# Performance work log

Measured on AMD Instinct MI355X. Metric: run time of the kernel, lower is better.

The kernel has to match this reference:

```python
import jax, jax.numpy as jnp
import numpy as np

DIM = 256
QK_DIM = 256
SCALE = QK_DIM ** (-0.5)


def depthwise_conv3x3(x_img, w, b):
    # x_img: [B, C, H, W], w: [C, 1, 3, 3] (OIHW, groups=C), b: [C]
    out = jax.lax.conv_general_dilated(
        x_img, w, window_strides=(1, 1), padding='SAME',
        feature_group_count=x_img.shape[1],
        dimension_numbers=('NCHW', 'OIHW', 'NCHW'))
    return out + b[None, :, None, None]


def setup_inputs() -> dict:
    key = jax.random.key(0)
    ks = jax.random.split(key, 7)
    B, N, C = 4, 4096, DIM
    s = 0.02
    return {
        'x': jax.random.normal(ks[0], (B, N, C), jnp.float32),
        'W_qkv': jax.random.normal(ks[1], (C, 3 * C), jnp.float32) * s,
        'W_gate': jax.random.normal(ks[2], (C, C), jnp.float32) * s,
        'b_gate': jax.random.normal(ks[3], (C,), jnp.float32) * s,
        'W_proj': jax.random.normal(ks[4], (C, C), jnp.float32) * s,
        'pe_w': jax.random.normal(ks[5], (C, 1, 3, 3), jnp.float32) * s,
        'pe_b': jax.random.normal(ks[6], (C,), jnp.float32) * s,
    }


def reference(x, W_qkv, W_gate, b_gate, W_proj, pe_w, pe_b):
    B, N, C = x.shape
    ws = int(N ** 0.5)
    qkv = x @ W_qkv                               # [B, N, 3C]
    q, k, v = jnp.split(qkv, [QK_DIM, 2 * QK_DIM], axis=-1)
    z = jax.nn.gelu(x @ W_gate + b_gate, approximate=False)  # [B, N, C]
    # depthwise-conv positional encoding on q viewed as an image
    q_img = jnp.transpose(q, (0, 2, 1)).reshape(B, C, ws, ws)
    pe = depthwise_conv3x3(q_img, pe_w, pe_b).reshape(B, C, N)
    pe = jnp.transpose(pe, (0, 2, 1))             # [B, N, C]
    # single-head attention (heads arg unused in the original forward)
    attn = jax.nn.softmax(jnp.einsum('bnc,bmc->bnm', q, k) * SCALE, axis=-1)
    out = jnp.einsum('bnm,bmc->bnc', attn, v) + pe
    out = out * z
    return out @ W_proj
```

## Files before the change

### kernel.cpp

```cpp
#include <hip/hip_runtime.h>
#include <hip/hip_bf16.h>
#include <math.h>
#include <stdint.h>

typedef unsigned short u16;
typedef __attribute__((ext_vector_type(8))) short bf8;
typedef __attribute__((ext_vector_type(4))) float f4;

#define SC_LOG2E 0.09016844f

__device__ __forceinline__ float b2f(u16 u) {
    union { uint32_t i; float f; } v; v.i = ((uint32_t)u) << 16; return v.f;
}
__device__ __forceinline__ u16 f2b(float f) {
    union { float f; uint32_t i; } v; v.f = f;
    uint32_t r = (v.i + 0x7FFFu + ((v.i >> 16) & 1u)) >> 16;
    return (u16)r;
}
__device__ __forceinline__ uint32_t pk_bf16(float lo, float hi) {
    uint32_t r;
    asm("v_cvt_pk_bf16_f32 %0, %1, %2" : "=v"(r) : "v"(lo), "v"(hi));
    return r;
}

__global__ __launch_bounds__(256) void prep_all(
        const float* __restrict__ Wqkv, const float* __restrict__ Wgate,
        const float* __restrict__ Wproj, const float* __restrict__ x,
        u16* __restrict__ WT_all, u16* __restrict__ WTp,
        u16* __restrict__ xb) {
    int bid = blockIdx.x;
    if (bid < 80) {
        __shared__ float tile[64][65];
        int t = threadIdx.x;
        int lid = (bid < 64) ? bid : (bid - 64);
        int n0 = (lid >> 2) * 64, k0 = (lid & 3) * 64;
        const float* src; int stride, ncol; u16* dst;
        if (bid < 64) {
            if (n0 < 768) { src = Wqkv; stride = 768; ncol = n0; }
            else          { src = Wgate; stride = 256; ncol = n0 - 768; }
            dst = WT_all;
        } else { src = Wproj; stride = 256; ncol = n0; dst = WTp; }
        int cr = t & 63, rr = t >> 6;
#pragma unroll
        for (int i = 0; i < 16; i++) {
            int r = rr * 16 + i;
            tile[r][cr] = src[(size_t)(k0 + r) * stride + ncol + cr];
        }
        __syncthreads();
#pragma unroll
        for (int i = 0; i < 16; i++) {
            int rw = rr * 16 + i;
            dst[(size_t)(n0 + rw) * 256 + k0 + cr] = f2b(tile[cr][rw]);
        }
    } else {
        int i = ((bid - 80) * 256 + threadIdx.x) * 4;
        float4 f = *(const float4*)&x[i];
        uint2 o;
        o.x = pk_bf16(f.x, f.y);
        o.y = pk_bf16(f.z, f.w);
        *(uint2*)&xb[i] = o;
    }
}

__global__ __launch_bounds__(512) void gemm_qkvz(
        const u16* __restrict__ xb, const u16* __restrict__ WT,
        const float* __restrict__ b_gate,
        u16* __restrict__ qo, u16* __restrict__ ko,
        u16* __restrict__ vT, u16* __restrict__ zo) {
    __shared__ u16 As[64 * 520];
    __shared__ u16 Bp[2][32 * 520];
    const int t = threadIdx.x;
    const int w = t >> 6, lane = t & 63, l15 = lane & 15, q4 = lane >> 4;
    const int m0 = blockIdx.x * 128;
    const int nb = blockIdx.y * 512;

    const int lo = lane >> 5;
    const int lcn = ((lane & 31) - 4 * lo) & 31;

    auto stageA = [&]() {
#pragma unroll
        for (int rr = 0; rr < 8; rr++) {
            int pp = rr * 8 + w;
            const u16* g = &xb[(size_t)(m0 + pp * 2 + lo) * 256 + lcn * 8];
            __builtin_amdgcn_global_load_lds(
                (const __attribute__((address_space(1))) unsigned int*)g,
                (__attribute__((address_space(3))) unsigned int*)&As[pp * 520],
                16, 0, 0);
        }
    };
    auto stageB = [&](int p, u16* dst) {
#pragma unroll
        for (int rr = 0; rr < 4; rr++) {
            int pp = rr * 8 + w;
            const u16* g = &WT[(size_t)(nb + p * 64 + pp * 2 + lo) * 256 + lcn * 8];
            __builtin_amdgcn_global_load_lds(
                (const __attribute__((address_space(1))) unsigned int*)g,
                (__attribute__((address_space(3))) unsigned int*)&dst[pp * 520],
                16, 0, 0);
        }
    };
    auto kaddr = [&](const u16* base, int row, int cn) -> const u16* {
        int o = row & 1;
        return base + (row >> 1) * 520 + o * 256 + (((cn + 4 * o) & 31) << 3);
    };

    stageA();
    stageB(0, Bp[0]);

    const int mtb = (w & 3) * 32;
    const int ntb = (w >> 2) * 32;

    for (int p = 0; p < 8; ++p) {
        __syncthreads();
        if (p < 7) stageB(p + 1, Bp[(p + 1) & 1]);
        const u16* Bs = Bp[p & 1];
        const int n0g = nb + p * 64;
        const int kind = n0g >> 8;
        const int pcol = n0g & 255;

        f4 acc[2][2];
#pragma unroll
        for (int i = 0; i < 2; i++)
#pragma unroll
            for (int j = 0; j < 2; j++) acc[i][j] = (f4){0.f, 0.f, 0.f, 0.f};

        __builtin_amdgcn_s_setprio(1);
#pragma unroll
        for (int c = 0; c < 8; c++) {
            bf8 af0 = *(const bf8*)kaddr(As, mtb + l15, c * 4 + q4);
            bf8 af1 = *(const bf8*)kaddr(As, mtb + 16 + l15, c * 4 + q4);
            bf8 bf0 = *(const bf8*)kaddr(Bs, ntb + l15, c * 4 + q4);
            bf8 bf1 = *(const bf8*)kaddr(Bs, ntb + 16 + l15, c * 4 + q4);
            if (kind == 2) {
                acc[0][0] = __builtin_amdgcn_mfma_f32_16x16x32_bf16(af0, bf0, acc[0][0], 0, 0, 0);
                acc[0][1] = __builtin_amdgcn_mfma_f32_16x16x32_bf16(af0, bf1, acc[0][1], 0, 0, 0);
                acc[1][0] = __builtin_amdgcn_mfma_f32_16x16x32_bf16(af1, bf0, acc[1][0], 0, 0, 0);
                acc[1][1] = __builtin_amdgcn_mfma_f32_16x16x32_bf16(af1, bf1, acc[1][1], 0, 0, 0);
            } else {
                acc[0][0] = __builtin_amdgcn_mfma_f32_16x16x32_bf16(bf0, af0, acc[0][0], 0, 0, 0);
                acc[0][1] = __builtin_amdgcn_mfma_f32_16x16x32_bf16(bf1, af0, acc[0][1], 0, 0, 0);
                acc[1][0] = __builtin_amdgcn_mfma_f32_16x16x32_bf16(bf0, af1, acc[1][0], 0, 0, 0);
                acc[1][1] = __builtin_amdgcn_mfma_f32_16x16x32_bf16(bf1, af1, acc[1][1], 0, 0, 0);
            }
        }
        __builtin_amdgcn_s_setprio(0);

        if (kind == 2) {
            int bb = m0 >> 12;
            int nnb = (m0 & 4095) + mtb + q4 * 4;
#pragma unroll
            for (int i = 0; i < 2; i++) {
                int nn = nnb + i * 16;
#pragma unroll
                for (int j = 0; j < 2; j++) {
                    int vc = pcol + ntb + j * 16 + l15;
                    uint2 pk;
                    pk.x = pk_bf16(acc[i][j][0], acc[i][j][1]);
                    pk.y = pk_bf16(acc[i][j][2], acc[i][j][3]);
                    *(uint2*)&vT[(size_t)(bb * 256 + vc) * 4096 + nn] = pk;
                }
            }
        } else if (kind == 3) {
#pragma unroll
            for (int i = 0; i < 2; i++) {
                size_t mrow = (size_t)(m0 + mtb + i * 16 + l15) * 256 + pcol;
#pragma unroll
                for (int j = 0; j < 2; j++) {
                    int col = ntb + j * 16 + q4 * 4;
                    float4 bg4 = *(const float4*)&b_gate[pcol + col];
                    float v0 = acc[i][j][0] + bg4.x;
                    float v1 = acc[i][j][1] + bg4.y;
                    float v2 = acc[i][j][2] + bg4.z;
                    float v3 = acc[i][j][3] + bg4.w;
                    v0 = 0.5f * v0 * (1.0f + erff(v0 * 0.70710678118654752f));
                    v1 = 0.5f * v1 * (1.0f + erff(v1 * 0.70710678118654752f));
                    v2 = 0.5f * v2 * (1.0f + erff(v2 * 0.70710678118654752f));
                    v3 = 0.5f * v3 * (1.0f + erff(v3 * 0.70710678118654752f));
                    uint2 o;
                    o.x = pk_bf16(v0, v1);
                    o.y = pk_bf16(v2, v3);
                    *(uint2*)&zo[mrow + col] = o;
                }
            }
        } else {
            u16* dst = (kind == 0) ? qo : ko;
#pragma unroll
            for (int i = 0; i < 2; i++) {
                size_t mrow = (size_t)(m0 + mtb + i * 16 + l15) * 256 + pcol;
#pragma unroll
                for (int j = 0; j < 2; j++) {
                    int col = ntb + j * 16 + q4 * 4;
                    uint2 o;
                    o.x = pk_bf16(acc[i][j][0], acc[i][j][1]);
                    o.y = pk_bf16(acc[i][j][2], acc[i][j][3]);
                    *(uint2*)&dst[mrow + col] = o;
                }
            }
        }
    }
}

__global__ __launch_bounds__(256) void conv_pe(
        const u16* __restrict__ q, const float* __restrict__ pw,
        const float* __restrict__ pb, u16* __restrict__ pe) {
    const int bid = blockIdx.x;
    const int b = bid >> 8, h = (bid >> 2) & 63, wsg = bid & 3;
    const int t = threadIdx.x;
    const int c4 = (t & 63) * 4;
    const int ws4 = t >> 6;
    const int w0 = wsg * 16 + ws4 * 4;

    float wf[36];
#pragma unroll
    for (int j = 0; j < 9; j++) {
        float4 v = *(const float4*)&pw[c4 * 9 + j * 4];
        wf[j * 4 + 0] = v.x; wf[j * 4 + 1] = v.y;
        wf[j * 4 + 2] = v.z; wf[j * 4 + 3] = v.w;
    }
    float4 bias4 = *(const float4*)&pb[c4];
    float bias[4] = {bias4.x, bias4.y, bias4.z, bias4.w};

    const u16* qb = q + b * (4096 * 256);
    u16* peb = pe + b * (4096 * 256);
    const bool vTop = h > 0, vBot = h < 63;

    float v[3][6][4];
#pragma unroll
    for (int j = 0; j < 6; j++) {
        int pos = w0 - 1 + j;
        bool inw = (pos >= 0) && (pos < 64);
#pragma unroll
        for (int r = 0; r < 3; r++) {
            bool ok = inw && ((r == 0) ? vTop : (r == 2) ? vBot : true);
            ushort4 u4 = {0, 0, 0, 0};
            if (ok) u4 = *(const ushort4*)&qb[((h - 1 + r) * 64 + pos) * 256 + c4];
            v[r][j][0] = b2f(u4.x); v[r][j][1] = b2f(u4.y);
            v[r][j][2] = b2f(u4.z); v[r][j][3] = b2f(u4.w);
        }
    }
#pragma unroll
    for (int w2 = 0; w2 < 4; w2++) {
        float o[4];
#pragma unroll
        for (int ch = 0; ch < 4; ch++) {
            float acc = bias[ch];
#pragma unroll
            for (int r = 0; r < 3; r++)
#pragma unroll
                for (int j = 0; j < 3; j++)
                    acc += wf[ch * 9 + r * 3 + j] * v[r][w2 + j][ch];
            o[ch] = acc;
        }
        uint2 st;
        st.x = pk_bf16(o[0], o[1]);
        st.y = pk_bf16(o[2], o[3]);
        *(uint2*)&peb[(h * 64 + w0 + w2) * 256 + c4] = st;
    }
}

__global__ __launch_bounds__(512) void attn(
        const u16* __restrict__ q, const u16* __restrict__ k,
        const u16* __restrict__ vT, const u16* __restrict__ pe,
        const u16* __restrict__ z, const u16* __restrict__ WTp,
        float* __restrict__ out) {
    __shared__ u16 Kst[32 * 520];
    __shared__ u16 Vs2[2][256 * 64];
    __shared__ u16 Ps[64 * 72];
    __shared__ float l_part[8][64];

    const int t = threadIdx.x;
    const int w = t >> 6, lane = t & 63, l15 = lane & 15, q4 = lane >> 4;
    const int kg = w >> 1, qh = w & 1;
    const int xcd = blockIdx.x & 7;
    const int b = xcd >> 1;
    const int qt = (blockIdx.x >> 3) * 2 + (xcd & 1);
    const int m0 = b * 4096 + qt * 64;

    const u16* kb = k + (size_t)b * 4096 * 256;
    const u16* vbase = vT + (size_t)b * 256 * 4096;

    const int lo = lane >> 5;
    const int lcn = ((lane & 31) - 4 * lo) & 31;

    auto stage64 = [&](const u16* src) {
#pragma unroll
        for (int rr = 0; rr < 4; rr++) {
            int pp = rr * 8 + w;
            const u16* g = src + (size_t)(pp * 2 + lo) * 256 + lcn * 8;
            u16* l = &Kst[pp * 520];
            __builtin_amdgcn_global_load_lds(
                (const __attribute__((address_space(1))) unsigned int*)g,
                (__attribute__((address_space(3))) unsigned int*)l, 16, 0, 0);
        }
    };
    const int vrl = lane >> 3, vsl = lane & 7;
    auto stageV = [&](const u16* src, u16* dst) {
#pragma unroll
        for (int j = 0; j < 4; j++) {
            int op = j * 8 + w;
            int r = op * 8 + vrl;
            int cn = (vsl - r) & 7;
            const u16* g = src + (size_t)r * 4096 + cn * 8;
            u16* l = dst + op * 512;
            __builtin_amdgcn_global_load_lds(
                (const __attribute__((address_space(1))) unsigned int*)g,
                (__attribute__((address_space(3))) unsigned int*)l, 16, 0, 0);
        }
    };
    auto kaddr = [&](int row, int cn) -> const u16* {
        int o = row & 1;
        return &Kst[(row >> 1) * 520 + o * 256 + (((cn + 4 * o) & 31) << 3)];
    };

    stage64(q + (size_t)m0 * 256);
    __syncthreads();
    bf8 qf[2][8];
#pragma unroll
    for (int qtt = 0; qtt < 2; qtt++)
#pragma unroll
        for (int c = 0; c < 8; c++)
            qf[qtt][c] = *(const bf8*)kaddr(qh * 32 + qtt * 16 + l15, c * 4 + q4);
    __syncthreads();

    stage64(kb);
    stageV(vbase, Vs2[0]);

    f4 O[2][4];
#pragma unroll
    for (int vg = 0; vg < 2; vg++)
#pragma unroll
        for (int qg = 0; qg < 4; qg++) O[vg][qg] = (f4){0.f, 0.f, 0.f, 0.f};
    float lrow[2] = {0.f, 0.f};

    auto body = [&](int kt, const u16* Vcur, u16* Vnxt) {
        __syncthreads();

        f4 St[2];
        St[0] = (f4){0.f, 0.f, 0.f, 0.f};
        St[1] = (f4){0.f, 0.f, 0.f, 0.f};
        __builtin_amdgcn_s_setprio(1);
#pragma unroll
        for (int c = 0; c < 8; c++) {
            bf8 kf = *(const bf8*)kaddr(kg * 16 + l15, c * 4 + q4);
            St[0] = __builtin_amdgcn_mfma_f32_16x16x32_bf16(kf, qf[0][c], St[0], 0, 0, 0);
            St[1] = __builtin_amdgcn_mfma_f32_16x16x32_bf16(kf, qf[1][c], St[1], 0, 0, 0);
        }
        __builtin_amdgcn_s_setprio(0);

#pragma unroll
        for (int qtt = 0; qtt < 2; qtt++) {
            float e0 = exp2f(fminf(fmaxf(St[qtt][0] * SC_LOG2E, -30.f), 30.f));
            float e1 = exp2f(fminf(fmaxf(St[qtt][1] * SC_LOG2E, -30.f), 30.f));
            float e2 = exp2f(fminf(fmaxf(St[qtt][2] * SC_LOG2E, -30.f), 30.f));
            float e3 = exp2f(fminf(fmaxf(St[qtt][3] * SC_LOG2E, -30.f), 30.f));
            uint2 pk;
            pk.x = pk_bf16(e0, e1);
            pk.y = pk_bf16(e2, e3);
            int qrow = qh * 32 + qtt * 16 + l15;
            *(uint2*)&Ps[qrow * 72 + kg * 16 + q4 * 4] = pk;
            float s = (e0 + e1) + (e2 + e3);
            s += __shfl_xor(s, 16);
            s += __shfl_xor(s, 32);
            lrow[qtt] += s;
        }
        __syncthreads();

        if (kt < 63) {
            stage64(kb + (size_t)(kt + 1) * 16384);
            stageV(vbase + (size_t)(kt + 1) * 64, Vnxt);
        }

        bf8 pf[4][2], vfr[2][2];
#pragma unroll
        for (int qg = 0; qg < 4; qg++)
#pragma unroll
            for (int kh = 0; kh < 2; kh++)
                pf[qg][kh] = *(bf8*)&Ps[(qg * 16 + l15) * 72 + kh * 32 + q4 * 8];
#pragma unroll
        for (int vg = 0; vg < 2; vg++)
#pragma unroll
            for (int kh = 0; kh < 2; kh++) {
                int R = w * 32 + vg * 16 + l15;
                int slot = ((kh * 4 + q4) + R) & 7;
                vfr[vg][kh] = *(const bf8*)&Vcur[R * 64 + slot * 8];
            }
        __builtin_amdgcn_s_setprio(1);
#pragma unroll
        for (int vg = 0; vg < 2; vg++)
#pragma unroll
            for (int qg = 0; qg < 4; qg++) {
                O[vg][qg] = __builtin_amdgcn_mfma_f32_16x16x32_bf16(
                    vfr[vg][0], pf[qg][0], O[vg][qg], 0, 0, 0);
                O[vg][qg] = __builtin_amdgcn_mfma_f32_16x16x32_bf16(
                    vfr[vg][1], pf[qg][1], O[vg][qg], 0, 0, 0);
            }
        __builtin_amdgcn_s_setprio(0);
    };

    for (int kt2 = 0; kt2 < 64; kt2 += 2) {
        body(kt2,     Vs2[0], Vs2[1]);
        body(kt2 + 1, Vs2[1], Vs2[0]);
    }

    if (q4 == 0) {
        l_part[w][qh * 32 + l15] = lrow[0];
        l_part[w][qh * 32 + 16 + l15] = lrow[1];
    }
    __syncthreads();

    u16* Us = Kst;
#pragma unroll
    for (int qg = 0; qg < 4; qg++) {
        int qrow = qg * 16 + l15;
        int qhq = qg >> 1;
        float lt = l_part[qhq][qrow] + l_part[2 + qhq][qrow]
                 + l_part[4 + qhq][qrow] + l_part[6 + qhq][qrow];
        float linv = 1.0f / lt;
        size_t mrow = (size_t)(m0 + qrow) * 256;
#pragma unroll
        for (int vg = 0; vg < 2; vg++) {
            int vcb = w * 32 + vg * 16 + q4 * 4;
            ushort4 pe4 = *(const ushort4*)&pe[mrow + vcb];
            ushort4 z4  = *(const ushort4*)&z[mrow + vcb];
            float r0 = (O[vg][qg][0] * linv + b2f(pe4.x)) * b2f(z4.x);
            float r1 = (O[vg][qg][1] * linv + b2f(pe4.y)) * b2f(z4.y);
            float r2 = (O[vg][qg][2] * linv + b2f(pe4.z)) * b2f(z4.z);
            float r3 = (O[vg][qg][3] * linv + b2f(pe4.w)) * b2f(z4.w);
            uint2 o4;
            o4.x = pk_bf16(r0, r1);
            o4.y = pk_bf16(r2, r3);
            int cn = vcb >> 3;
            int slot = (cn + qrow) & 31;
            *(uint2*)&Us[qrow * 256 + slot * 8 + (vcb & 7)] = o4;
        }
    }

    auto stageW = [&](const u16* src, u16* dst) {
#pragma unroll
        for (int j = 0; j < 4; j++) {
            int op = j * 8 + w;
            int r = op * 2 + lo;
            int cn = ((lane & 31) - r) & 31;
            const u16* g = src + (size_t)r * 256 + cn * 8;
            __builtin_amdgcn_global_load_lds(
                (const __attribute__((address_space(1))) unsigned int*)g,
                (__attribute__((address_space(3))) unsigned int*)&dst[op * 512],
                16, 0, 0);
        }
    };

    stageW(WTp, (u16*)Vs2[0]);
    __syncthreads();

    const int mtl = (w & 3) * 16;
    const int ntl = (w >> 2) * 32;
#pragma unroll
    for (int nq = 0; nq < 4; nq++) {
        if (nq < 3) stageW(WTp + (size_t)(nq + 1) * 64 * 256, (u16*)Vs2[(nq + 1) & 1]);
        const u16* Wl = (const u16*)Vs2[nq & 1];
        f4 a0 = (f4){0.f, 0.f, 0.f, 0.f};
        f4 a1 = (f4){0.f, 0.f, 0.f, 0.f};
        const int mrowL = mtl + l15;
        const int ln0 = ntl + l15, ln1 = ntl + 16 + l15;
        __builtin_amdgcn_s_setprio(1);
#pragma unroll
        for (int c = 0; c < 8; c++) {
            int cc = c * 4 + q4;
            bf8 af = *(const bf8*)&Us[mrowL * 256 + (((cc + mrowL) & 31) << 3)];
            bf8 b0 = *(const bf8*)&Wl[ln0 * 256 + (((cc + ln0) & 31) << 3)];
            bf8 b1 = *(const bf8*)&Wl[ln1 * 256 + (((cc + ln1) & 31) << 3)];
            a0 = __builtin_amdgcn_mfma_f32_16x16x32_bf16(b0, af, a0, 0, 0, 0);
            a1 = __builtin_amdgcn_mfma_f32_16x16x32_bf16(b1, af, a1, 0, 0, 0);
        }
        __builtin_amdgcn_s_setprio(0);
        float* ob = &out[(size_t)(m0 + mrowL) * 256 + nq * 64 + ntl];
        *(f4*)&ob[q4 * 4] = a0;
        *(f4*)&ob[16 + q4 * 4] = a1;
        __syncthreads();
    }
}

extern "C" void kernel_launch(void* const* d_in, const int* in_sizes, int n_in,
                              void* d_out, int out_size, void* d_ws, size_t ws_size,
                              hipStream_t stream) {
    (void)in_sizes; (void)n_in; (void)out_size; (void)ws_size;
    const float* x      = (const float*)d_in[0];
    const float* Wqkv   = (const float*)d_in[1];
    const float* Wgate  = (const float*)d_in[2];
    const float* bgate  = (const float*)d_in[3];
    const float* Wproj  = (const float*)d_in[4];
    const float* pw     = (const float*)d_in[5];
    const float* pb     = (const float*)d_in[6];
    float* out = (float*)d_out;

    char* ws = (char*)d_ws;
    u16* WT_all = (u16*)(ws);
    u16* WTp    = (u16*)(ws + 524288);
    u16* q      = (u16*)(ws + 655360);
    u16* k      = (u16*)(ws + 9043968);
    u16* vT     = (u16*)(ws + 17432576);
    u16* z      = (u16*)(ws + 25821184);
    u16* pe     = (u16*)(ws + 34209792);
    u16* xb     = (u16*)(ws + 42598400);

    prep_all<<<4176, 256, 0, stream>>>(Wqkv, Wgate, Wproj, x, WT_all, WTp, xb);
    gemm_qkvz<<<dim3(128, 2), 512, 0, stream>>>(xb, WT_all, bgate, q, k, vT, z);
    conv_pe<<<1024, 256, 0, stream>>>(q, pw, pb, pe);
    attn<<<256, 512, 0, stream>>>(q, k, vT, pe, z, WTp, out);
}
```

Measured before the change: 224.3 us.

## Fuse depthwise conv positional encoding into attention epilogue and defer row-sum reduction

Removes the separate conv_pe kernel and its pe buffer round trip. The attention epilogue now computes the 3x3 depthwise conv directly from q, reading neighbours from global memory. The softmax denominator shuffle reduction moves out of the inner loop and runs once at the end. The exp clamp to [-30,30] is also dropped, which saves ALU work but risks overflow if scores grow large. The epilogue does more scattered global loads and uses more registers.

```diff
diff --git a/kernel.cpp b/kernel.cpp
--- a/kernel.cpp
+++ b/kernel.cpp
@@ -200,69 +200,11 @@
     }
 }
 
-__global__ __launch_bounds__(256) void conv_pe(
-        const u16* __restrict__ q, const float* __restrict__ pw,
-        const float* __restrict__ pb, u16* __restrict__ pe) {
-    const int bid = blockIdx.x;
-    const int b = bid >> 8, h = (bid >> 2) & 63, wsg = bid & 3;
-    const int t = threadIdx.x;
-    const int c4 = (t & 63) * 4;
-    const int ws4 = t >> 6;
-    const int w0 = wsg * 16 + ws4 * 4;
-
-    float wf[36];
-#pragma unroll
-    for (int j = 0; j < 9; j++) {
-        float4 v = *(const float4*)&pw[c4 * 9 + j * 4];
-        wf[j * 4 + 0] = v.x; wf[j * 4 + 1] = v.y;
-        wf[j * 4 + 2] = v.z; wf[j * 4 + 3] = v.w;
-    }
-    float4 bias4 = *(const float4*)&pb[c4];
-    float bias[4] = {bias4.x, bias4.y, bias4.z, bias4.w};
-
-    const u16* qb = q + b * (4096 * 256);
-    u16* peb = pe + b * (4096 * 256);
-    const bool vTop = h > 0, vBot = h < 63;
-
-    float v[3][6][4];
-#pragma unroll
-    for (int j = 0; j < 6; j++) {
-        int pos = w0 - 1 + j;
-        bool inw = (pos >= 0) && (pos < 64);
-#pragma unroll
-        for (int r = 0; r < 3; r++) {
-            bool ok = inw && ((r == 0) ? vTop : (r == 2) ? vBot : true);
-            ushort4 u4 = {0, 0, 0, 0};
-            if (ok) u4 = *(const ushort4*)&qb[((h - 1 + r) * 64 + pos) * 256 + c4];
-            v[r][j][0] = b2f(u4.x); v[r][j][1] = b2f(u4.y);
-            v[r][j][2] = b2f(u4.z); v[r][j][3] = b2f(u4.w);
-        }
-    }
-#pragma unroll
-    for (int w2 = 0; w2 < 4; w2++) {
-        float o[4];
-#pragma unroll
-        for (int ch = 0; ch < 4; ch++) {
-            float acc = bias[ch];
-#pragma unroll
-            for (int r = 0; r < 3; r++)
-#pragma unroll
-                for (int j = 0; j < 3; j++)
-                    acc += wf[ch * 9 + r * 3 + j] * v[r][w2 + j][ch];
-            o[ch] = acc;
-        }
-        uint2 st;
-        st.x = pk_bf16(o[0], o[1]);
-        st.y = pk_bf16(o[2], o[3]);
-        *(uint2*)&peb[(h * 64 + w0 + w2) * 256 + c4] = st;
-    }
-}
-
 __global__ __launch_bounds__(512) void attn(
         const u16* __restrict__ q, const u16* __restrict__ k,
-        const u16* __restrict__ vT, const u16* __restrict__ pe,
-        const u16* __restrict__ z, const u16* __restrict__ WTp,
-        float* __restrict__ out) {
+        const u16* __restrict__ vT, const float* __restrict__ pw,
+        const float* __restrict__ pb, const u16* __restrict__ z,
+        const u16* __restrict__ WTp, float* __restrict__ out) {
     __shared__ u16 Kst[32 * 520];
     __shared__ u16 Vs2[2][256 * 64];
     __shared__ u16 Ps[64 * 72];
@@ -349,19 +291,16 @@
 
 #pragma unroll
         for (int qtt = 0; qtt < 2; qtt++) {
-            float e0 = exp2f(fminf(fmaxf(St[qtt][0] * SC_LOG2E, -30.f), 30.f));
-            float e1 = exp2f(fminf(fmaxf(St[qtt][1] * SC_LOG2E, -30.f), 30.f));
-            float e2 = exp2f(fminf(fmaxf(St[qtt][2] * SC_LOG2E, -30.f), 30.f));
-            float e3 = exp2f(fminf(fmaxf(St[qtt][3] * SC_LOG2E, -30.f), 30.f));
+            float e0 = exp2f(St[qtt][0] * SC_LOG2E);
+            float e1 = exp2f(St[qtt][1] * SC_LOG2E);
+            float e2 = exp2f(St[qtt][2] * SC_LOG2E);
+            float e3 = exp2f(St[qtt][3] * SC_LOG2E);
             uint2 pk;
             pk.x = pk_bf16(e0, e1);
             pk.y = pk_bf16(e2, e3);
             int qrow = qh * 32 + qtt * 16 + l15;
             *(uint2*)&Ps[qrow * 72 + kg * 16 + q4 * 4] = pk;
-            float s = (e0 + e1) + (e2 + e3);
-            s += __shfl_xor(s, 16);
-            s += __shfl_xor(s, 32);
-            lrow[qtt] += s;
+            lrow[qtt] += (e0 + e1) + (e2 + e3);
         }
         __syncthreads();
 
@@ -402,6 +341,13 @@
         body(kt2 + 1, Vs2[1], Vs2[0]);
     }
 
+#pragma unroll
+    for (int qtt = 0; qtt < 2; qtt++) {
+        float s = lrow[qtt];
+        s += __shfl_xor(s, 16);
+        s += __shfl_xor(s, 32);
+        lrow[qtt] = s;
+    }
     if (q4 == 0) {
         l_part[w][qh * 32 + l15] = lrow[0];
         l_part[w][qh * 32 + 16 + l15] = lrow[1];
@@ -409,29 +355,55 @@
     __syncthreads();
 
     u16* Us = Kst;
-#pragma unroll
-    for (int qg = 0; qg < 4; qg++) {
-        int qrow = qg * 16 + l15;
-        int qhq = qg >> 1;
-        float lt = l_part[qhq][qrow] + l_part[2 + qhq][qrow]
-                 + l_part[4 + qhq][qrow] + l_part[6 + qhq][qrow];
-        float linv = 1.0f / lt;
-        size_t mrow = (size_t)(m0 + qrow) * 256;
-#pragma unroll
-        for (int vg = 0; vg < 2; vg++) {
-            int vcb = w * 32 + vg * 16 + q4 * 4;
-            ushort4 pe4 = *(const ushort4*)&pe[mrow + vcb];
-            ushort4 z4  = *(const ushort4*)&z[mrow + vcb];
-            float r0 = (O[vg][qg][0] * linv + b2f(pe4.x)) * b2f(z4.x);
-            float r1 = (O[vg][qg][1] * linv + b2f(pe4.y)) * b2f(z4.y);
-            float r2 = (O[vg][qg][2] * linv + b2f(pe4.z)) * b2f(z4.z);
-            float r3 = (O[vg][qg][3] * linv + b2f(pe4.w)) * b2f(z4.w);
+    const u16* qb2 = q + (size_t)b * 4096 * 256;
+    const bool hT = qt > 0, hB = qt < 63;
+#pragma unroll
+    for (int vg = 0; vg < 2; vg++) {
+        const int c4 = w * 32 + vg * 16 + q4 * 4;
+        float wf[36];
+#pragma unroll
+        for (int j9 = 0; j9 < 9; j9++) {
+            float4 v4 = *(const float4*)&pw[c4 * 9 + j9 * 4];
+            wf[j9 * 4 + 0] = v4.x; wf[j9 * 4 + 1] = v4.y;
+            wf[j9 * 4 + 2] = v4.z; wf[j9 * 4 + 3] = v4.w;
+        }
+        float4 b4 = *(const float4*)&pb[c4];
+#pragma unroll
+        for (int qg = 0; qg < 4; qg++) {
+            int qrow = qg * 16 + l15;
+            int qhq = qg >> 1;
+            float lt = l_part[qhq][qrow] + l_part[2 + qhq][qrow]
+                     + l_part[4 + qhq][qrow] + l_part[6 + qhq][qrow];
+            float linv = 1.0f / lt;
+            float a0 = b4.x, a1 = b4.y, a2 = b4.z, a3 = b4.w;
+#pragma unroll
+            for (int r = 0; r < 3; r++) {
+                if ((r == 0 && !hT) || (r == 2 && !hB)) continue;
+                int hh = qt - 1 + r;
+#pragma unroll
+                for (int j = 0; j < 3; j++) {
+                    int ww = qrow - 1 + j;
+                    if (ww >= 0 && ww < 64) {
+                        ushort4 u4 = *(const ushort4*)&qb2[((hh << 6) + ww) * 256 + c4];
+                        a0 += wf[0 + r * 3 + j] * b2f(u4.x);
+                        a1 += wf[9 + r * 3 + j] * b2f(u4.y);
+                        a2 += wf[18 + r * 3 + j] * b2f(u4.z);
+                        a3 += wf[27 + r * 3 + j] * b2f(u4.w);
+                    }
+                }
+            }
+            size_t mrow = (size_t)(m0 + qrow) * 256;
+            ushort4 z4 = *(const ushort4*)&z[mrow + c4];
+            float r0 = (O[vg][qg][0] * linv + a0) * b2f(z4.x);
+            float r1 = (O[vg][qg][1] * linv + a1) * b2f(z4.y);
+            float r2 = (O[vg][qg][2] * linv + a2) * b2f(z4.z);
+            float r3 = (O[vg][qg][3] * linv + a3) * b2f(z4.w);
             uint2 o4;
             o4.x = pk_bf16(r0, r1);
             o4.y = pk_bf16(r2, r3);
-            int cn = vcb >> 3;
+            int cn = c4 >> 3;
             int slot = (cn + qrow) & 31;
-            *(uint2*)&Us[qrow * 256 + slot * 8 + (vcb & 7)] = o4;
+            *(uint2*)&Us[qrow * 256 + slot * 8 + (c4 & 7)] = o4;
         }
     }
 
@@ -500,11 +472,9 @@
     u16* k      = (u16*)(ws + 9043968);
     u16* vT     = (u16*)(ws + 17432576);
     u16* z      = (u16*)(ws + 25821184);
-    u16* pe     = (u16*)(ws + 34209792);
-    u16* xb     = (u16*)(ws + 42598400);
+    u16* xb     = (u16*)(ws + 34209792);
 
     prep_all<<<4176, 256, 0, stream>>>(Wqkv, Wgate, Wproj, x, WT_all, WTp, xb);
     gemm_qkvz<<<dim3(128, 2), 512, 0, stream>>>(xb, WT_all, bgate, q, k, vT, z);
-    conv_pe<<<1024, 256, 0, stream>>>(q, pw, pb, pe);
-    attn<<<256, 512, 0, stream>>>(q, k, vT, pe, z, WTp, out);
-}
+    attn<<<256, 512, 0, stream>>>(q, k, vT, pw, pb, z, WTp, out);
+}
```

After: 228.3 us. No clear change (+1.8%).
